# Optimization experiments

Measured on AMD Instinct MI355X. Metric: run time of the kernel, lower is better.

## Reference

```python
import jax, jax.numpy as jnp
import numpy as np

B, S, D, H = 4, 2048, 1024, 16
HD = D // H  # head dim = 64

def setup_inputs() -> dict:
    key = jax.random.key(0)
    k1, k2, k3 = jax.random.split(key, 3)
    x = jax.random.normal(k1, (B, S, D), dtype=jnp.float32)
    W_attn = jax.random.normal(k2, (D, 3 * D), dtype=jnp.float32) * 0.02
    b_attn = jnp.zeros((3 * D,), dtype=jnp.float32)
    W_proj = jax.random.normal(k3, (D, D), dtype=jnp.float32) * 0.02
    b_proj = jnp.zeros((D,), dtype=jnp.float32)
    return {"x": x, "W_attn": W_attn, "b_attn": b_attn, "W_proj": W_proj, "b_proj": b_proj}

def reference(x, W_attn, b_attn, W_proj, b_proj):
    b, s, d = x.shape
    qkv = x @ W_attn + b_attn                       # [b, s, 3d]
    q, k, v = jnp.split(qkv, 3, axis=-1)
    # [b, s, d] -> [b, h, s, hd]
    def heads(t):
        return t.reshape(b, s, H, HD).transpose(0, 2, 1, 3)
    q, k, v = heads(q), heads(k), heads(v)
    scale = 1.0 / jnp.sqrt(jnp.asarray(HD, dtype=x.dtype))
    scores = jnp.einsum('bhqd,bhkd->bhqk', q, k) * scale  # [b, h, s, s]
    causal = jnp.tril(jnp.ones((s, s), dtype=bool))
    scores = jnp.where(causal[None, None, :, :], scores, jnp.asarray(-jnp.inf, dtype=x.dtype))
    attn = jax.nn.softmax(scores, axis=-1)
    out = jnp.einsum('bhqk,bhkd->bhqd', attn, v)    # [b, h, s, hd]
    out = out.transpose(0, 2, 1, 3).reshape(b, s, d)
    return out @ W_proj + b_proj
```

## Files before the change

kernel.cpp:

```cpp
#include <hip/hip_runtime.h>
#include <hip/hip_bf16.h>
#include <stdint.h>

#define B_  4
#define S_  2048
#define D_  1024
#define H_  16
#define HD_ 64

typedef __attribute__((ext_vector_type(8))) short          s16x8;
typedef __attribute__((ext_vector_type(4))) float          f32x4;
typedef __attribute__((ext_vector_type(8))) unsigned short u16x8;

__device__ __forceinline__ unsigned short f2bf(float f) {
  union { float f; unsigned int u; } v; v.f = f;
  unsigned int u = v.u;
  u += 0x7fffu + ((u >> 16) & 1u);
  return (unsigned short)(u >> 16);
}

__global__ void k_cvt(const float* __restrict__ src, unsigned short* __restrict__ dst, int n4) {
  int i = blockIdx.x * blockDim.x + threadIdx.x;
  int stride = gridDim.x * blockDim.x;
  for (int j = i; j < n4; j += stride) {
    float4 v = reinterpret_cast<const float4*>(src)[j];
    ushort4 o;
    o.x = f2bf(v.x); o.y = f2bf(v.y); o.z = f2bf(v.z); o.w = f2bf(v.w);
    reinterpret_cast<ushort4*>(dst)[j] = o;
  }
}

__global__ void k_tpose_cvt(const float* __restrict__ src, unsigned short* __restrict__ dst,
                            int R, int C) {
  __shared__ unsigned short tile[64][72];
  int c0 = blockIdx.x * 64, r0 = blockIdx.y * 64;
  int tx = threadIdx.x & 63, ty = threadIdx.x >> 6;
#pragma unroll
  for (int i = 0; i < 16; ++i) {
    int r = ty * 16 + i;
    tile[r][tx] = f2bf(src[(size_t)(r0 + r) * C + c0 + tx]);
  }
  __syncthreads();
#pragma unroll
  for (int i = 0; i < 16; ++i) {
    int c = ty * 16 + i;
    dst[(size_t)(c0 + c) * R + r0 + tx] = tile[tx][c];
  }
}

__global__ void k_tpose_v(const unsigned short* __restrict__ src, unsigned short* __restrict__ dst) {
  __shared__ unsigned short tile[64][72];
  int s0 = blockIdx.x * 64, bh = blockIdx.y;
  int tx = threadIdx.x & 63, ty = threadIdx.x >> 6;
  const unsigned short* sb = src + (size_t)bh * S_ * HD_;
  unsigned short*       db = dst + (size_t)bh * S_ * HD_;
#pragma unroll
  for (int i = 0; i < 16; ++i) {
    int r = ty * 16 + i;
    tile[r][tx] = sb[(size_t)(s0 + r) * HD_ + tx];
  }
  __syncthreads();
#pragma unroll
  for (int i = 0; i < 16; ++i) {
    int hd = ty * 16 + i;
    db[(size_t)hd * S_ + s0 + tx] = tile[tx][hd];
  }
}

__device__ __forceinline__ void gemm_core(const unsigned short* __restrict__ A,
                                          const unsigned short* __restrict__ Bt,
                                          int K, int m0, int n0,
                                          unsigned short* sm, f32x4 acc[4][4]) {
  const int t = threadIdx.x;
  const int w = t >> 6, l = t & 63;
  const int wm = w >> 1, wn = w & 1;
  const int lo = l & 15, hi = l >> 4;

  const int ci0 = t, ci1 = t + 256;
  const int r0c = ci0 >> 2, o0c = ci0 & 3;
  const int r1c = ci1 >> 2, o1c = ci1 & 3;
  const int swz0 = r0c * 32 + ((o0c ^ ((r0c >> 1) & 3)) << 3);
  const int swz1 = r1c * 32 + ((o1c ^ ((r1c >> 1) & 3)) << 3);
  const unsigned short* gA0 = A  + (size_t)(m0 + r0c) * K + o0c * 8;
  const unsigned short* gA1 = A  + (size_t)(m0 + r1c) * K + o1c * 8;
  const unsigned short* gB0 = Bt + (size_t)(n0 + r0c) * K + o0c * 8;
  const unsigned short* gB1 = Bt + (size_t)(n0 + r1c) * K + o1c * 8;

#pragma unroll
  for (int m = 0; m < 4; ++m)
#pragma unroll
    for (int n = 0; n < 4; ++n)
      acc[m][n] = (f32x4){0.f, 0.f, 0.f, 0.f};

  const int NT = K >> 5;
  u16x8 ra0 = *(const u16x8*)gA0, ra1 = *(const u16x8*)gA1;
  u16x8 rb0 = *(const u16x8*)gB0, rb1 = *(const u16x8*)gB1;

  for (int kt = 0; kt < NT; ++kt) {
    unsigned short* buf = sm + (kt & 1) * 8192;
    if (kt) __syncthreads();
    *(u16x8*)(buf + swz0)        = ra0;
    *(u16x8*)(buf + swz1)        = ra1;
    *(u16x8*)(buf + 4096 + swz0) = rb0;
    *(u16x8*)(buf + 4096 + swz1) = rb1;
    if (kt + 1 < NT) {
      int k0 = (kt + 1) << 5;
      ra0 = *(const u16x8*)(gA0 + k0);
      ra1 = *(const u16x8*)(gA1 + k0);
      rb0 = *(const u16x8*)(gB0 + k0);
      rb1 = *(const u16x8*)(gB1 + k0);
    }
    __syncthreads();
    const unsigned short* Ab = buf;
    const unsigned short* Bb = buf + 4096;
    s16x8 af[4], bfr[4];
#pragma unroll
    for (int m = 0; m < 4; ++m) {
      int row = wm * 64 + m * 16 + lo;
      af[m] = *(const s16x8*)(Ab + row * 32 + ((hi ^ ((row >> 1) & 3)) << 3));
    }
#pragma unroll
    for (int n = 0; n < 4; ++n) {
      int row = wn * 64 + n * 16 + lo;
      bfr[n] = *(const s16x8*)(Bb + row * 32 + ((hi ^ ((row >> 1) & 3)) << 3));
    }
    __builtin_amdgcn_s_setprio(1);
#pragma unroll
    for (int m = 0; m < 4; ++m)
#pragma unroll
      for (int n = 0; n < 4; ++n)
        acc[m][n] = __builtin_amdgcn_mfma_f32_16x16x32_bf16(af[m], bfr[n], acc[m][n], 0, 0, 0);
    __builtin_amdgcn_s_setprio(0);
  }
}

__global__ __launch_bounds__(256, 2)
void k_gemm_qkv(const unsigned short* __restrict__ A, const unsigned short* __restrict__ Bt,
                const float* __restrict__ bias,
                unsigned short* __restrict__ Qh, unsigned short* __restrict__ Kh,
                unsigned short* __restrict__ Vh) {
  __shared__ unsigned short sm[2 * 8192];
  const int m0 = blockIdx.y * 128, n0 = blockIdx.x * 128;
  f32x4 acc[4][4];
  gemm_core(A, Bt, 1024, m0, n0, sm, acc);
  const int t = threadIdx.x, w = t >> 6, l = t & 63;
  const int wm = w >> 1, wn = w & 1, lo = l & 15, hi = l >> 4;
#pragma unroll
  for (int m = 0; m < 4; ++m)
#pragma unroll
    for (int n = 0; n < 4; ++n) {
      int col = n0 + wn * 64 + n * 16 + lo;
      float bv = bias[col];
      int sel = col >> 10, cw = col & 1023, h = cw >> 6, hd = cw & 63;
      float scl = (sel == 0) ? 0.18033688011112042f : 1.0f;
      unsigned short* dst = (sel == 0) ? Qh : ((sel == 1) ? Kh : Vh);
#pragma unroll
      for (int r = 0; r < 4; ++r) {
        int row = m0 + wm * 64 + m * 16 + hi * 4 + r;
        int b = row >> 11, s = row & 2047;
        dst[(((size_t)b * H_ + h) * S_ + s) * HD_ + hd] = f2bf((acc[m][n][r] + bv) * scl);
      }
    }
}

__global__ __launch_bounds__(256, 2)
void k_gemm_proj(const unsigned short* __restrict__ A, const unsigned short* __restrict__ Bt,
                 const float* __restrict__ bias, float* __restrict__ C, int N) {
  __shared__ unsigned short sm[2 * 8192];
  const int m0 = blockIdx.y * 128, n0 = blockIdx.x * 128;
  f32x4 acc[4][4];
  gemm_core(A, Bt, 1024, m0, n0, sm, acc);
  const int t = threadIdx.x, w = t >> 6, l = t & 63;
  const int wm = w >> 1, wn = w & 1, lo = l & 15, hi = l >> 4;
#pragma unroll
  for (int m = 0; m < 4; ++m)
#pragma unroll
    for (int n = 0; n < 4; ++n) {
      int col = n0 + wn * 64 + n * 16 + lo;
      float bv = bias[col];
#pragma unroll
      for (int r = 0; r < 4; ++r) {
        int row = m0 + wm * 64 + m * 16 + hi * 4 + r;
        C[(size_t)row * N + col] = acc[m][n][r] + bv;
      }
    }
}

__global__ __launch_bounds__(256, 2)
void k_attn(const unsigned short* __restrict__ Qh, const unsigned short* __restrict__ Kh,
            const unsigned short* __restrict__ Vt, unsigned short* __restrict__ ctx) {
  __shared__ unsigned short Kl[4096];
  __shared__ unsigned short Vl[4096];
  const int bh = blockIdx.y;
  const int t = threadIdx.x, w = t >> 6, l = t & 63, lo = l & 15, hi = l >> 4;
  const unsigned short* Qb = Qh + (size_t)bh * S_ * HD_;
  const unsigned short* Kb = Kh + (size_t)bh * S_ * HD_;
  const unsigned short* Vb = Vt + (size_t)bh * S_ * HD_;
  const int bb = bh >> 4, h = bh & 15;

  const int r0s = t >> 3, schunk = t & 7;
  const int r1s = r0s + 32;
  const int ks0 = (r0s & 32) | ((r0s & 1) << 4) | ((r0s >> 1) & 15);
  const int ks1 = (r1s & 32) | ((r1s & 1) << 4) | ((r1s >> 1) & 15);
  unsigned short* kdst0 = &Kl[ks0 * 64 + 8 * (schunk ^ (ks0 & 7))];
  unsigned short* kdst1 = &Kl[ks1 * 64 + 8 * (schunk ^ (ks1 & 7))];
  unsigned short* vdst0 = &Vl[r0s * 64 + 8 * (schunk ^ (r0s & 7))];
  unsigned short* vdst1 = &Vl[r1s * 64 + 8 * (schunk ^ (r1s & 7))];
  const unsigned short* ksrc0 = Kb + r0s * HD_ + schunk * 8;
  const unsigned short* ksrc1 = Kb + r1s * HD_ + schunk * 8;
  const unsigned short* vsrc0 = Vb + (size_t)r0s * S_ + schunk * 8;
  const unsigned short* vsrc1 = Vb + (size_t)r1s * S_ + schunk * 8;

  for (int half = 0; half < 2; ++half) {
    const int iq = half ? (15 - (int)blockIdx.x) : (int)blockIdx.x;
    const int q0 = iq * 128;
    const int nt = (q0 >> 6) + 2;

    s16x8 qf[2][2];
    int qbase[2];
#pragma unroll
    for (int g = 0; g < 2; ++g) {
      qbase[g] = q0 + g * 64 + w * 16;
#pragma unroll
      for (int kk = 0; kk < 2; ++kk)
        qf[g][kk] = *(const s16x8*)(Qb + (size_t)(qbase[g] + lo) * HD_ + kk * 32 + hi * 8);
    }
    f32x4 O[2][4];
#pragma unroll
    for (int g = 0; g < 2; ++g)
#pragma unroll
      for (int nh = 0; nh < 4; ++nh) O[g][nh] = (f32x4){0.f, 0.f, 0.f, 0.f};
    float mrun[2] = {-1e30f, -1e30f}, lrun[2] = {0.f, 0.f};

    u16x8 rk0 = *(const u16x8*)ksrc0, rk1 = *(const u16x8*)ksrc1;
    u16x8 rv0 = *(const u16x8*)vsrc0, rv1 = *(const u16x8*)vsrc1;

    for (int kt = 0; kt < nt; ++kt) {
      const int kv0 = kt * 64;
      __syncthreads();
      *(u16x8*)kdst0 = rk0;
      *(u16x8*)kdst1 = rk1;
      *(u16x8*)vdst0 = rv0;
      *(u16x8*)vdst1 = rv1;
      if (kt + 1 < nt) {
        rk0 = *(const u16x8*)(ksrc0 + (size_t)(kv0 + 64) * HD_);
        rk1 = *(const u16x8*)(ksrc1 + (size_t)(kv0 + 64) * HD_);
        rv0 = *(const u16x8*)(vsrc0 + kv0 + 64);
        rv1 = *(const u16x8*)(vsrc1 + kv0 + 64);
      }
      __syncthreads();

      f32x4 p[2][4];
#pragma unroll
      for (int g = 0; g < 2; ++g)
#pragma unroll
        for (int n = 0; n < 4; ++n) p[g][n] = (f32x4){0.f, 0.f, 0.f, 0.f};
#pragma unroll
      for (int kk = 0; kk < 2; ++kk) {
        s16x8 kf[4];
#pragma unroll
        for (int n = 0; n < 4; ++n)
          kf[n] = *(const s16x8*)&Kl[(n * 16 + lo) * 64 + 8 * ((kk * 4 + hi) ^ (lo & 7))];
        __builtin_amdgcn_s_setprio(1);
#pragma unroll
        for (int g = 0; g < 2; ++g)
#pragma unroll
          for (int n = 0; n < 4; ++n)
            p[g][n] = __builtin_amdgcn_mfma_f32_16x16x32_bf16(kf[n], qf[g][kk], p[g][n], 0, 0, 0);
        __builtin_amdgcn_s_setprio(0);
      }

      union PU { unsigned int u[4]; s16x8 s; };
      PU pa[2][2];
#pragma unroll
      for (int g = 0; g < 2; ++g) {
        if (kv0 + 63 > qbase[g]) {
          const int q = qbase[g] + lo;
#pragma unroll
          for (int n = 0; n < 4; ++n)
#pragma unroll
            for (int r = 0; r < 4; ++r) {
              int kv = kv0 + 32 * (n >> 1) + 8 * hi + 2 * r + (n & 1);
              p[g][n][r] = (kv <= q) ? p[g][n][r] : -1e30f;
            }
        }
        float mx = fmaxf(fmaxf(fmaxf(p[g][0][0], p[g][0][1]), fmaxf(p[g][0][2], p[g][0][3])),
                         fmaxf(fmaxf(p[g][1][0], p[g][1][1]), fmaxf(p[g][1][2], p[g][1][3])));
        mx = fmaxf(mx, fmaxf(fmaxf(fmaxf(p[g][2][0], p[g][2][1]), fmaxf(p[g][2][2], p[g][2][3])),
                             fmaxf(fmaxf(p[g][3][0], p[g][3][1]), fmaxf(p[g][3][2], p[g][3][3]))));
        mx = fmaxf(mx, __shfl_xor(mx, 16));
        mx = fmaxf(mx, __shfl_xor(mx, 32));
        float mnew = fmaxf(mrun[g], mx);
        float alpha = exp2f(mrun[g] - mnew);
        mrun[g] = mnew;
        float sum = 0.f;
#pragma unroll
        for (int n = 0; n < 4; ++n)
#pragma unroll
          for (int r = 0; r < 4; ++r) {
            float e = exp2f(p[g][n][r] - mnew);
            p[g][n][r] = e;
            sum += e;
          }
        sum += __shfl_xor(sum, 16);
        sum += __shfl_xor(sum, 32);
        lrun[g] = lrun[g] * alpha + sum;
#pragma unroll
        for (int r = 0; r < 4; ++r) {
          float ar_ = __shfl(alpha, 4 * hi + r);
#pragma unroll
          for (int nh = 0; nh < 4; ++nh) O[g][nh][r] *= ar_;
        }
#pragma unroll
        for (int c = 0; c < 2; ++c)
#pragma unroll
          for (int r = 0; r < 4; ++r) {
            unsigned int pk;
            asm("v_cvt_pk_bf16_f32 %0, %1, %2"
                : "=v"(pk) : "v"(p[g][2 * c][r]), "v"(p[g][2 * c + 1][r]));
            pa[g][c].u[r] = pk;
          }
      }

#pragma unroll
      for (int c = 0; c < 2; ++c) {
        s16x8 vf[4];
#pragma unroll
        for (int nh = 0; nh < 4; ++nh)
          vf[nh] = *(const s16x8*)&Vl[(nh * 16 + lo) * 64 + 8 * ((4 * c + hi) ^ (lo & 7))];
        __builtin_amdgcn_s_setprio(1);
#pragma unroll
        for (int nh = 0; nh < 4; ++nh) {
          O[0][nh] = __builtin_amdgcn_mfma_f32_16x16x32_bf16(pa[0][c].s, vf[nh], O[0][nh], 0, 0, 0);
          O[1][nh] = __builtin_amdgcn_mfma_f32_16x16x32_bf16(pa[1][c].s, vf[nh], O[1][nh], 0, 0, 0);
        }
        __builtin_amdgcn_s_setprio(0);
      }
    }

#pragma unroll
    for (int g = 0; g < 2; ++g) {
#pragma unroll
      for (int r = 0; r < 4; ++r) {
        float li = 1.0f / __shfl(lrun[g], 4 * hi + r);
        int qg = qbase[g] + 4 * hi + r;
#pragma unroll
        for (int nh = 0; nh < 4; ++nh) {
          int hd = nh * 16 + lo;
          ctx[(((size_t)(bb * S_ + qg)) * H_ + h) * HD_ + hd] = f2bf(O[g][nh][r] * li);
        }
      }
    }
  }
}

extern "C" void kernel_launch(void* const* d_in, const int* in_sizes, int n_in,
                              void* d_out, int out_size, void* d_ws, size_t ws_size,
                              hipStream_t stream) {
  const float* x      = (const float*)d_in[0];
  const float* W_attn = (const float*)d_in[1];
  const float* b_attn = (const float*)d_in[2];
  const float* W_proj = (const float*)d_in[3];
  const float* b_proj = (const float*)d_in[4];
  float* out = (float*)d_out;

  char* ws = (char*)d_ws;
  size_t off = 0;
  auto alloc = [&](size_t bytes) {
    char* p = ws + off;
    off += (bytes + 255) & ~(size_t)255;
    return p;
  };
  unsigned short* xb  = (unsigned short*)alloc((size_t)8192 * 1024 * 2);
  unsigned short* Wta = (unsigned short*)alloc((size_t)3072 * 1024 * 2);
  unsigned short* Wtp = (unsigned short*)alloc((size_t)1024 * 1024 * 2);
  unsigned short* Qh  = (unsigned short*)alloc((size_t)64 * 2048 * 64 * 2);
  unsigned short* Kh  = (unsigned short*)alloc((size_t)64 * 2048 * 64 * 2);
  unsigned short* Vh  = (unsigned short*)alloc((size_t)64 * 2048 * 64 * 2);
  unsigned short* Vt  = (unsigned short*)alloc((size_t)64 * 2048 * 64 * 2);
  unsigned short* ctx = (unsigned short*)alloc((size_t)8192 * 1024 * 2);

  k_cvt<<<dim3(2048), dim3(256), 0, stream>>>(x, xb, (8192 * 1024) / 4);
  k_tpose_cvt<<<dim3(48, 16), dim3(256), 0, stream>>>(W_attn, Wta, 1024, 3072);
  k_tpose_cvt<<<dim3(16, 16), dim3(256), 0, stream>>>(W_proj, Wtp, 1024, 1024);
  k_gemm_qkv<<<dim3(24, 64), dim3(256), 0, stream>>>(xb, Wta, b_attn, Qh, Kh, Vh);
  k_tpose_v<<<dim3(32, 64), dim3(256), 0, stream>>>(Vh, Vt);
  k_attn<<<dim3(8, 64), dim3(256), 0, stream>>>(Qh, Kh, Vt, ctx);
  k_gemm_proj<<<dim3(8, 64), dim3(256), 0, stream>>>(ctx, Wtp, b_proj, out, 1024);
}
```

Baseline: 195.8 us.

## Run both causal query halves concurrently in 512-thread attention blocks with lazy rescale

The attention kernel now launches 512 threads per block. Two groups of four waves each process one of the paired query tiles (iq and 15-iq) at the same time, sharing K/V tiles staged once into LDS, instead of looping over the halves one after another. Waves whose query tile needs fewer KV tiles skip the compute but still join the barriers. The online softmax also skips the running-max rescale when the new max stays within 8 of the old one. The GEMM launch bounds rise to 3 blocks per CU, which may limit registers and cause spills.

Result: slower. 210.9 us (+7.7%).

```diff
diff --git a/kernel.cpp b/kernel.cpp
--- a/kernel.cpp
+++ b/kernel.cpp
@@ -134,7 +134,7 @@
   }
 }
 
-__global__ __launch_bounds__(256, 2)
+__global__ __launch_bounds__(256, 3)
 void k_gemm_qkv(const unsigned short* __restrict__ A, const unsigned short* __restrict__ Bt,
                 const float* __restrict__ bias,
                 unsigned short* __restrict__ Qh, unsigned short* __restrict__ Kh,
@@ -163,7 +163,7 @@
     }
 }
 
-__global__ __launch_bounds__(256, 2)
+__global__ __launch_bounds__(256, 3)
 void k_gemm_proj(const unsigned short* __restrict__ A, const unsigned short* __restrict__ Bt,
                  const float* __restrict__ bias, float* __restrict__ C, int N) {
   __shared__ unsigned short sm[2 * 8192];
@@ -186,169 +186,164 @@
     }
 }
 
-__global__ __launch_bounds__(256, 2)
+__global__ __launch_bounds__(512, 4)
 void k_attn(const unsigned short* __restrict__ Qh, const unsigned short* __restrict__ Kh,
             const unsigned short* __restrict__ Vt, unsigned short* __restrict__ ctx) {
   __shared__ unsigned short Kl[4096];
   __shared__ unsigned short Vl[4096];
   const int bh = blockIdx.y;
   const int t = threadIdx.x, w = t >> 6, l = t & 63, lo = l & 15, hi = l >> 4;
+  const int wg = w >> 2, wi = w & 3;
   const unsigned short* Qb = Qh + (size_t)bh * S_ * HD_;
   const unsigned short* Kb = Kh + (size_t)bh * S_ * HD_;
   const unsigned short* Vb = Vt + (size_t)bh * S_ * HD_;
   const int bb = bh >> 4, h = bh & 15;
 
-  const int r0s = t >> 3, schunk = t & 7;
-  const int r1s = r0s + 32;
-  const int ks0 = (r0s & 32) | ((r0s & 1) << 4) | ((r0s >> 1) & 15);
-  const int ks1 = (r1s & 32) | ((r1s & 1) << 4) | ((r1s >> 1) & 15);
-  unsigned short* kdst0 = &Kl[ks0 * 64 + 8 * (schunk ^ (ks0 & 7))];
-  unsigned short* kdst1 = &Kl[ks1 * 64 + 8 * (schunk ^ (ks1 & 7))];
-  unsigned short* vdst0 = &Vl[r0s * 64 + 8 * (schunk ^ (r0s & 7))];
-  unsigned short* vdst1 = &Vl[r1s * 64 + 8 * (schunk ^ (r1s & 7))];
-  const unsigned short* ksrc0 = Kb + r0s * HD_ + schunk * 8;
-  const unsigned short* ksrc1 = Kb + r1s * HD_ + schunk * 8;
-  const unsigned short* vsrc0 = Vb + (size_t)r0s * S_ + schunk * 8;
-  const unsigned short* vsrc1 = Vb + (size_t)r1s * S_ + schunk * 8;
-
-  for (int half = 0; half < 2; ++half) {
-    const int iq = half ? (15 - (int)blockIdx.x) : (int)blockIdx.x;
-    const int q0 = iq * 128;
-    const int nt = (q0 >> 6) + 2;
-
-    s16x8 qf[2][2];
-    int qbase[2];
+  const int srow = t >> 3, schunk = t & 7;
+  const int ks = (srow & 32) | ((srow & 1) << 4) | ((srow >> 1) & 15);
+  unsigned short* kdst = &Kl[ks   * 64 + 8 * (schunk ^ (ks   & 7))];
+  unsigned short* vdst = &Vl[srow * 64 + 8 * (schunk ^ (srow & 7))];
+  const unsigned short* ksrc = Kb + srow * HD_ + schunk * 8;
+  const unsigned short* vsrc = Vb + (size_t)srow * S_ + schunk * 8;
+
+  const int iq = wg ? (15 - (int)blockIdx.x) : (int)blockIdx.x;
+  const int q0 = iq * 128;
+  const int myNt = (q0 >> 6) + 2;
+  const int nt = 32 - 2 * (int)blockIdx.x;
+
+  s16x8 qf[2][2];
+  int qbase[2];
+#pragma unroll
+  for (int g = 0; g < 2; ++g) {
+    qbase[g] = q0 + g * 64 + wi * 16;
+#pragma unroll
+    for (int kk = 0; kk < 2; ++kk)
+      qf[g][kk] = *(const s16x8*)(Qb + (size_t)(qbase[g] + lo) * HD_ + kk * 32 + hi * 8);
+  }
+  f32x4 O[2][4];
+#pragma unroll
+  for (int g = 0; g < 2; ++g)
+#pragma unroll
+    for (int nh = 0; nh < 4; ++nh) O[g][nh] = (f32x4){0.f, 0.f, 0.f, 0.f};
+  float mrun[2] = {-1e30f, -1e30f}, lrun[2] = {0.f, 0.f};
+
+  u16x8 rk = *(const u16x8*)ksrc;
+  u16x8 rv = *(const u16x8*)vsrc;
+
+  for (int kt = 0; kt < nt; ++kt) {
+    const int kv0 = kt * 64;
+    __syncthreads();
+    *(u16x8*)kdst = rk;
+    *(u16x8*)vdst = rv;
+    if (kt + 1 < nt) {
+      rk = *(const u16x8*)(ksrc + (size_t)(kv0 + 64) * HD_);
+      rv = *(const u16x8*)(vsrc + kv0 + 64);
+    }
+    __syncthreads();
+    if (kt >= myNt) continue;
+
+    f32x4 p[2][4];
+#pragma unroll
+    for (int g = 0; g < 2; ++g)
+#pragma unroll
+      for (int n = 0; n < 4; ++n) p[g][n] = (f32x4){0.f, 0.f, 0.f, 0.f};
+#pragma unroll
+    for (int kk = 0; kk < 2; ++kk) {
+      s16x8 kf[4];
+#pragma unroll
+      for (int n = 0; n < 4; ++n)
+        kf[n] = *(const s16x8*)&Kl[(n * 16 + lo) * 64 + 8 * ((kk * 4 + hi) ^ (lo & 7))];
+      __builtin_amdgcn_s_setprio(1);
+#pragma unroll
+      for (int g = 0; g < 2; ++g)
+#pragma unroll
+        for (int n = 0; n < 4; ++n)
+          p[g][n] = __builtin_amdgcn_mfma_f32_16x16x32_bf16(kf[n], qf[g][kk], p[g][n], 0, 0, 0);
+      __builtin_amdgcn_s_setprio(0);
+    }
+
+    union PU { unsigned int u[4]; s16x8 s; };
+    PU pa[2][2];
 #pragma unroll
     for (int g = 0; g < 2; ++g) {
-      qbase[g] = q0 + g * 64 + w * 16;
-#pragma unroll
-      for (int kk = 0; kk < 2; ++kk)
-        qf[g][kk] = *(const s16x8*)(Qb + (size_t)(qbase[g] + lo) * HD_ + kk * 32 + hi * 8);
-    }
-    f32x4 O[2][4];
-#pragma unroll
-    for (int g = 0; g < 2; ++g)
-#pragma unroll
-      for (int nh = 0; nh < 4; ++nh) O[g][nh] = (f32x4){0.f, 0.f, 0.f, 0.f};
-    float mrun[2] = {-1e30f, -1e30f}, lrun[2] = {0.f, 0.f};
-
-    u16x8 rk0 = *(const u16x8*)ksrc0, rk1 = *(const u16x8*)ksrc1;
-    u16x8 rv0 = *(const u16x8*)vsrc0, rv1 = *(const u16x8*)vsrc1;
-
-    for (int kt = 0; kt < nt; ++kt) {
-      const int kv0 = kt * 64;
-      __syncthreads();
-      *(u16x8*)kdst0 = rk0;
-      *(u16x8*)kdst1 = rk1;
-      *(u16x8*)vdst0 = rv0;
-      *(u16x8*)vdst1 = rv1;
-      if (kt + 1 < nt) {
-        rk0 = *(const u16x8*)(ksrc0 + (size_t)(kv0 + 64) * HD_);
-        rk1 = *(const u16x8*)(ksrc1 + (size_t)(kv0 + 64) * HD_);
-        rv0 = *(const u16x8*)(vsrc0 + kv0 + 64);
-        rv1 = *(const u16x8*)(vsrc1 + kv0 + 64);
-      }
-      __syncthreads();
-
-      f32x4 p[2][4];
-#pragma unroll
-      for (int g = 0; g < 2; ++g)
-#pragma unroll
-        for (int n = 0; n < 4; ++n) p[g][n] = (f32x4){0.f, 0.f, 0.f, 0.f};
-#pragma unroll
-      for (int kk = 0; kk < 2; ++kk) {
-        s16x8 kf[4];
+      if (kv0 + 63 > qbase[g]) {
+        const int q = qbase[g] + lo;
 #pragma unroll
         for (int n = 0; n < 4; ++n)
-          kf[n] = *(const s16x8*)&Kl[(n * 16 + lo) * 64 + 8 * ((kk * 4 + hi) ^ (lo & 7))];
-        __builtin_amdgcn_s_setprio(1);
-#pragma unroll
-        for (int g = 0; g < 2; ++g)
-#pragma unroll
-          for (int n = 0; n < 4; ++n)
-            p[g][n] = __builtin_amdgcn_mfma_f32_16x16x32_bf16(kf[n], qf[g][kk], p[g][n], 0, 0, 0);
-        __builtin_amdgcn_s_setprio(0);
-      }
-
-      union PU { unsigned int u[4]; s16x8 s; };
-      PU pa[2][2];
-#pragma unroll
-      for (int g = 0; g < 2; ++g) {
-        if (kv0 + 63 > qbase[g]) {
-          const int q = qbase[g] + lo;
-#pragma unroll
-          for (int n = 0; n < 4; ++n)
-#pragma unroll
-            for (int r = 0; r < 4; ++r) {
-              int kv = kv0 + 32 * (n >> 1) + 8 * hi + 2 * r + (n & 1);
-              p[g][n][r] = (kv <= q) ? p[g][n][r] : -1e30f;
-            }
-        }
-        float mx = fmaxf(fmaxf(fmaxf(p[g][0][0], p[g][0][1]), fmaxf(p[g][0][2], p[g][0][3])),
-                         fmaxf(fmaxf(p[g][1][0], p[g][1][1]), fmaxf(p[g][1][2], p[g][1][3])));
-        mx = fmaxf(mx, fmaxf(fmaxf(fmaxf(p[g][2][0], p[g][2][1]), fmaxf(p[g][2][2], p[g][2][3])),
-                             fmaxf(fmaxf(p[g][3][0], p[g][3][1]), fmaxf(p[g][3][2], p[g][3][3]))));
-        mx = fmaxf(mx, __shfl_xor(mx, 16));
-        mx = fmaxf(mx, __shfl_xor(mx, 32));
+#pragma unroll
+          for (int r = 0; r < 4; ++r) {
+            int kv = kv0 + 32 * (n >> 1) + 8 * hi + 2 * r + (n & 1);
+            p[g][n][r] = (kv <= q) ? p[g][n][r] : -1e30f;
+          }
+      }
+      float mx = fmaxf(fmaxf(fmaxf(p[g][0][0], p[g][0][1]), fmaxf(p[g][0][2], p[g][0][3])),
+                       fmaxf(fmaxf(p[g][1][0], p[g][1][1]), fmaxf(p[g][1][2], p[g][1][3])));
+      mx = fmaxf(mx, fmaxf(fmaxf(fmaxf(p[g][2][0], p[g][2][1]), fmaxf(p[g][2][2], p[g][2][3])),
+                           fmaxf(fmaxf(p[g][3][0], p[g][3][1]), fmaxf(p[g][3][2], p[g][3][3]))));
+      mx = fmaxf(mx, __shfl_xor(mx, 16));
+      mx = fmaxf(mx, __shfl_xor(mx, 32));
+      const bool need = !__all(mx <= mrun[g] + 8.0f);
+      if (need) {
         float mnew = fmaxf(mrun[g], mx);
         float alpha = exp2f(mrun[g] - mnew);
         mrun[g] = mnew;
-        float sum = 0.f;
-#pragma unroll
-        for (int n = 0; n < 4; ++n)
-#pragma unroll
-          for (int r = 0; r < 4; ++r) {
-            float e = exp2f(p[g][n][r] - mnew);
-            p[g][n][r] = e;
-            sum += e;
-          }
-        sum += __shfl_xor(sum, 16);
-        sum += __shfl_xor(sum, 32);
-        lrun[g] = lrun[g] * alpha + sum;
+        lrun[g] *= alpha;
 #pragma unroll
         for (int r = 0; r < 4; ++r) {
           float ar_ = __shfl(alpha, 4 * hi + r);
 #pragma unroll
           for (int nh = 0; nh < 4; ++nh) O[g][nh][r] *= ar_;
         }
-#pragma unroll
-        for (int c = 0; c < 2; ++c)
-#pragma unroll
-          for (int r = 0; r < 4; ++r) {
-            unsigned int pk;
-            asm("v_cvt_pk_bf16_f32 %0, %1, %2"
-                : "=v"(pk) : "v"(p[g][2 * c][r]), "v"(p[g][2 * c + 1][r]));
-            pa[g][c].u[r] = pk;
-          }
-      }
-
-#pragma unroll
-      for (int c = 0; c < 2; ++c) {
-        s16x8 vf[4];
-#pragma unroll
-        for (int nh = 0; nh < 4; ++nh)
-          vf[nh] = *(const s16x8*)&Vl[(nh * 16 + lo) * 64 + 8 * ((4 * c + hi) ^ (lo & 7))];
-        __builtin_amdgcn_s_setprio(1);
-#pragma unroll
-        for (int nh = 0; nh < 4; ++nh) {
-          O[0][nh] = __builtin_amdgcn_mfma_f32_16x16x32_bf16(pa[0][c].s, vf[nh], O[0][nh], 0, 0, 0);
-          O[1][nh] = __builtin_amdgcn_mfma_f32_16x16x32_bf16(pa[1][c].s, vf[nh], O[1][nh], 0, 0, 0);
+      }
+      float sum = 0.f;
+#pragma unroll
+      for (int n = 0; n < 4; ++n)
+#pragma unroll
+        for (int r = 0; r < 4; ++r) {
+          float e = exp2f(p[g][n][r] - mrun[g]);
+          p[g][n][r] = e;
+          sum += e;
         }
-        __builtin_amdgcn_s_setprio(0);
-      }
-    }
-
-#pragma unroll
-    for (int g = 0; g < 2; ++g) {
-#pragma unroll
-      for (int r = 0; r < 4; ++r) {
-        float li = 1.0f / __shfl(lrun[g], 4 * hi + r);
-        int qg = qbase[g] + 4 * hi + r;
-#pragma unroll
-        for (int nh = 0; nh < 4; ++nh) {
-          int hd = nh * 16 + lo;
-          ctx[(((size_t)(bb * S_ + qg)) * H_ + h) * HD_ + hd] = f2bf(O[g][nh][r] * li);
+      sum += __shfl_xor(sum, 16);
+      sum += __shfl_xor(sum, 32);
+      lrun[g] += sum;
+#pragma unroll
+      for (int c = 0; c < 2; ++c)
+#pragma unroll
+        for (int r = 0; r < 4; ++r) {
+          unsigned int pk;
+          asm("v_cvt_pk_bf16_f32 %0, %1, %2"
+              : "=v"(pk) : "v"(p[g][2 * c][r]), "v"(p[g][2 * c + 1][r]));
+          pa[g][c].u[r] = pk;
         }
+    }
+
+#pragma unroll
+    for (int c = 0; c < 2; ++c) {
+      s16x8 vf[4];
+#pragma unroll
+      for (int nh = 0; nh < 4; ++nh)
+        vf[nh] = *(const s16x8*)&Vl[(nh * 16 + lo) * 64 + 8 * ((4 * c + hi) ^ (lo & 7))];
+      __builtin_amdgcn_s_setprio(1);
+#pragma unroll
+      for (int nh = 0; nh < 4; ++nh) {
+        O[0][nh] = __builtin_amdgcn_mfma_f32_16x16x32_bf16(pa[0][c].s, vf[nh], O[0][nh], 0, 0, 0);
+        O[1][nh] = __builtin_amdgcn_mfma_f32_16x16x32_bf16(pa[1][c].s, vf[nh], O[1][nh], 0, 0, 0);
+      }
+      __builtin_amdgcn_s_setprio(0);
+    }
+  }
+
+#pragma unroll
+  for (int g = 0; g < 2; ++g) {
+#pragma unroll
+    for (int r = 0; r < 4; ++r) {
+      float li = 1.0f / __shfl(lrun[g], 4 * hi + r);
+      int qg = qbase[g] + 4 * hi + r;
+#pragma unroll
+      for (int nh = 0; nh < 4; ++nh) {
+        int hd = nh * 16 + lo;
+        ctx[(((size_t)(bb * S_ + qg)) * H_ + h) * HD_ + hd] = f2bf(O[g][nh][r] * li);
       }
     }
   }
@@ -385,6 +380,6 @@
   k_tpose_cvt<<<dim3(16, 16), dim3(256), 0, stream>>>(W_proj, Wtp, 1024, 1024);
   k_gemm_qkv<<<dim3(24, 64), dim3(256), 0, stream>>>(xb, Wta, b_attn, Qh, Kh, Vh);
   k_tpose_v<<<dim3(32, 64), dim3(256), 0, stream>>>(Vh, Vt);
-  k_attn<<<dim3(8, 64), dim3(256), 0, stream>>>(Qh, Kh, Vt, ctx);
+  k_attn<<<dim3(8, 64), dim3(512), 0, stream>>>(Qh, Kh, Vt, ctx);
   k_gemm_proj<<<dim3(8, 64), dim3(256), 0, stream>>>(ctx, Wtp, b_proj, out, 1024);
 }
```
